# Kernel tuning notes

Hardware: AMD Instinct MI355X
Metric: run time of the kernel (lower is better)

Reference implementation:

```python
import jax, jax.numpy as jnp
import numpy as np

NUM_EMBEDDINGS = 1024
EMBEDDING_DIM = 256
COMMITMENT_COST = 0.25


def setup_inputs() -> dict:
    key = jax.random.key(0)
    k1, k2 = jax.random.split(key)
    z_e = jax.random.normal(k1, (32, 256, 32, 32), dtype=jnp.float32)
    # nn.init.uniform_(weight, -1/K, 1/K)
    bound = 1.0 / NUM_EMBEDDINGS
    weight = jax.random.uniform(k2, (NUM_EMBEDDINGS, EMBEDDING_DIM), dtype=jnp.float32,
                                minval=-bound, maxval=bound)
    return {"z_e": z_e, "weight": weight}


def reference(z_e, weight):
    B, C, H, W = z_e.shape
    sg = jax.lax.stop_gradient
    # (B, H, W, C) -> (N, C)
    flat = jnp.transpose(z_e, (0, 2, 3, 1)).reshape(-1, C)
    # squared L2 distances to each codebook vector: (N, K)
    dist = (jnp.sum(flat * flat, axis=1, keepdims=True)
            - 2.0 * flat @ weight.T
            + jnp.sum(weight * weight, axis=1))
    indices = jnp.argmin(dist, axis=1)  # (N,)
    # codebook lookup (equivalent to one-hot @ weight)
    quantized = weight[indices].reshape(B, H, W, C)
    quantized = jnp.transpose(quantized, (0, 3, 1, 2))  # (B, C, H, W)
    e_latent = jnp.mean((sg(quantized) - z_e) ** 2)
    q_latent = jnp.mean((quantized - sg(z_e)) ** 2)
    loss = q_latent + COMMITMENT_COST * e_latent
    # straight-through estimator
    quantized_st = z_e + sg(quantized - z_e)
    # codebook usage perplexity: avg_probs = mean of one-hot encodings
    n = flat.shape[0]
    counts = jax.ops.segment_sum(jnp.ones((n,), dtype=z_e.dtype), indices,
                                 num_segments=NUM_EMBEDDINGS)
    avg_probs = counts / n
    perplexity = jnp.exp(-jnp.sum(avg_probs * jnp.log(avg_probs + 1e-10)))
    return (quantized_st, loss, perplexity)
```

## Files before the change

### kernel.cpp

```cpp
#include <hip/hip_runtime.h>
#include <float.h>
#include <math.h>
#include <stdint.h>


#define NB   32
#define NC   256
#define NHW  1024
#define NK   1024
#define NELEM (NB*NC*NHW)

typedef __attribute__((ext_vector_type(8))) short bf16x8;
typedef __attribute__((ext_vector_type(4))) float f32x4;

__device__ __forceinline__ unsigned short f2bf(float f) {
    unsigned u = __float_as_uint(f);
    u += 0x7FFFu + ((u >> 16) & 1u);
    return (unsigned short)(u >> 16);
}

__global__ __launch_bounds__(256) void vq_prep(const float* __restrict__ w,
                                               unsigned short* __restrict__ cb,
                                               float* __restrict__ wsq,
                                               unsigned int* __restrict__ counts,
                                               float* __restrict__ loss_sum) {
    __shared__ float swsq[4][16];
    const int t   = blockIdx.x;
    const int tid = threadIdx.x;
    float sq = 0.f;
#pragma unroll
    for (int rep = 0; rep < 2; ++rep) {
        const int p = tid + rep * 256;
        const int cc = p >> 6, l = p & 63;
        const int n = l & 15, quad = l >> 4;
        const float* src = w + (t * 16 + n) * NC + cc * 32 + quad * 8;
        const float4 f0 = *(const float4*)src;
        const float4 f1 = *(const float4*)(src + 4);
        union { unsigned short u[8]; uint4 v; } pk;
        pk.u[0] = f2bf(-2.f * f0.x); pk.u[1] = f2bf(-2.f * f0.y);
        pk.u[2] = f2bf(-2.f * f0.z); pk.u[3] = f2bf(-2.f * f0.w);
        pk.u[4] = f2bf(-2.f * f1.x); pk.u[5] = f2bf(-2.f * f1.y);
        pk.u[6] = f2bf(-2.f * f1.z); pk.u[7] = f2bf(-2.f * f1.w);
        *(uint4*)(cb + (size_t)t * 4096 + cc * 512 + l * 8) = pk.v;
        sq = fmaf(f0.x, f0.x, sq); sq = fmaf(f0.y, f0.y, sq);
        sq = fmaf(f0.z, f0.z, sq); sq = fmaf(f0.w, f0.w, sq);
        sq = fmaf(f1.x, f1.x, sq); sq = fmaf(f1.y, f1.y, sq);
        sq = fmaf(f1.z, f1.z, sq); sq = fmaf(f1.w, f1.w, sq);
    }
    sq += __shfl_xor(sq, 16, 64);
    sq += __shfl_xor(sq, 32, 64);
    const int wv = tid >> 6, lane = tid & 63;
    if (lane < 16) swsq[wv][lane] = sq;
    __syncthreads();
    if (tid < 16)
        wsq[t * 16 + tid] = swsq[0][tid] + swsq[1][tid] + swsq[2][tid] + swsq[3][tid];
    if (t == 0) {
        for (int i = tid; i < NK; i += 256) counts[i] = 0u;
        if (tid == 0) loss_sum[0] = 0.f;
    }
}

__global__ __launch_bounds__(256, 2) void vq_dist(const float* __restrict__ z,
                                                  const float* __restrict__ wsq,
                                                  const unsigned short* __restrict__ cb,
                                                  unsigned int* __restrict__ counts,
                                                  int* __restrict__ gfidx) {
    __shared__ float sval[4][64];
    __shared__ int   sidx[4][64];

    const int tid  = threadIdx.x;
    const int wv   = tid >> 6;
    const int lane = tid & 63;
    const int n    = lane & 15;
    const int quad = lane >> 4;
    const int bid  = blockIdx.x;
    const int b    = bid >> 4;
    const int hw0  = (bid & 15) << 6;

    const float* zb = z + (size_t)b * (NC * NHW);

    bf16x8 bfr[4][8];
#pragma unroll
    for (int nt = 0; nt < 4; ++nt) {
#pragma unroll
        for (int cc = 0; cc < 8; ++cc) {
            const float* zp = zb + (size_t)(cc * 32 + quad * 8) * NHW + hw0 + nt * 16 + n;
            union { unsigned short u[8]; bf16x8 v; } pk;
#pragma unroll
            for (int j = 0; j < 8; ++j) pk.u[j] = f2bf(zp[(size_t)j * NHW]);
            bfr[nt][cc] = pk.v;
        }
    }

    float bv[4] = {FLT_MAX, FLT_MAX, FLT_MAX, FLT_MAX};
    int   bi[4] = {0, 0, 0, 0};
    const unsigned short* ap0 = cb + (size_t)(wv * 16) * 4096 + lane * 8;

    for (int mt = 0; mt < 16; ++mt) {
        const int kt = wv * 256 + mt * 16;
        const unsigned short* ap = ap0 + (size_t)mt * 4096;
        const f32x4 w4 = *(const f32x4*)(wsq + kt + quad * 4);
        f32x4 acc[4];
#pragma unroll
        for (int nt = 0; nt < 4; ++nt) acc[nt] = w4;
#pragma unroll
        for (int cc = 0; cc < 8; ++cc) {
            const bf16x8 af = *(const bf16x8*)(ap + cc * 512);
            acc[0] = __builtin_amdgcn_mfma_f32_16x16x32_bf16(af, bfr[0][cc], acc[0], 0, 0, 0);
            acc[1] = __builtin_amdgcn_mfma_f32_16x16x32_bf16(af, bfr[1][cc], acc[1], 0, 0, 0);
            acc[2] = __builtin_amdgcn_mfma_f32_16x16x32_bf16(af, bfr[2][cc], acc[2], 0, 0, 0);
            acc[3] = __builtin_amdgcn_mfma_f32_16x16x32_bf16(af, bfr[3][cc], acc[3], 0, 0, 0);
        }
#pragma unroll
        for (int nt = 0; nt < 4; ++nt) {
#pragma unroll
            for (int r = 0; r < 4; ++r) {
                const float v = acc[nt][r];
                if (v < bv[nt]) { bv[nt] = v; bi[nt] = kt + quad * 4 + r; }
            }
        }
    }

#pragma unroll
    for (int nt = 0; nt < 4; ++nt) {
#pragma unroll
        for (int off = 16; off <= 32; off <<= 1) {
            const float ov = __shfl_xor(bv[nt], off, 64);
            const int   ok = __shfl_xor(bi[nt], off, 64);
            if (ov < bv[nt] || (ov == bv[nt] && ok < bi[nt])) { bv[nt] = ov; bi[nt] = ok; }
        }
    }
    if (lane < 16) {
#pragma unroll
        for (int nt = 0; nt < 4; ++nt) {
            sval[wv][nt * 16 + lane] = bv[nt];
            sidx[wv][nt * 16 + lane] = bi[nt];
        }
    }
    __syncthreads();

    if (tid < 64) {
        float bestv = sval[0][tid];
        int   besti = sidx[0][tid];
#pragma unroll
        for (int q = 1; q < 4; ++q) {
            const float v = sval[q][tid];
            const int   k = sidx[q][tid];
            if (v < bestv || (v == bestv && k < besti)) { bestv = v; besti = k; }
        }
        gfidx[b * NHW + hw0 + tid] = besti;
        atomicAdd(&counts[besti], 1u);
    }
}

__global__ __launch_bounds__(256, 4) void vq_scatter(const float* __restrict__ z,
                                                     const float* __restrict__ w,
                                                     const int* __restrict__ gfidx,
                                                     float* __restrict__ loss_sum,
                                                     float* __restrict__ out) {
    __shared__ float lred[4];
    const int tid = threadIdx.x;
    const int bid = blockIdx.x;
    const int b   = bid >> 5;
    const int c0  = (bid & 31) << 3;
    const int hw4 = tid << 2;

    const int4 k4 = *(const int4*)(gfidx + b * NHW + hw4);
    const float* zb = z   + (size_t)b * (NC * NHW);
    float*       ob = out + (size_t)b * (NC * NHW);

    float lsum = 0.f;
#pragma unroll
    for (int i = 0; i < 8; ++i) {
        const int c = c0 + i;
        const float4 zq = *(const float4*)(zb + (size_t)c * NHW + hw4);
        float4 q;
        q.x = w[k4.x * NC + c];
        q.y = w[k4.y * NC + c];
        q.z = w[k4.z * NC + c];
        q.w = w[k4.w * NC + c];
        float d;
        d = q.x - zq.x; lsum = fmaf(d, d, lsum);
        d = q.y - zq.y; lsum = fmaf(d, d, lsum);
        d = q.z - zq.z; lsum = fmaf(d, d, lsum);
        d = q.w - zq.w; lsum = fmaf(d, d, lsum);
        *(float4*)(ob + (size_t)c * NHW + hw4) = q;
    }
#pragma unroll
    for (int off = 32; off; off >>= 1) lsum += __shfl_down(lsum, off, 64);
    const int lane = tid & 63, wv = tid >> 6;
    if (lane == 0) lred[wv] = lsum;
    __syncthreads();
    if (tid == 0)
        atomicAdd(loss_sum, lred[0] + lred[1] + lred[2] + lred[3]);
}

__global__ __launch_bounds__(256) void vq_final(const unsigned int* __restrict__ counts,
                                                const float* __restrict__ loss_sum,
                                                float* __restrict__ out) {
    __shared__ float red[4];
    const int tid = threadIdx.x;
    float s = 0.f;
#pragma unroll
    for (int p = 0; p < 4; ++p) {
        const float pr = (float)counts[tid + p * 256] * (1.f / 32768.f);
        s = fmaf(pr, logf(pr + 1e-10f), s);
    }
#pragma unroll
    for (int off = 32; off; off >>= 1) s += __shfl_down(s, off, 64);
    if ((tid & 63) == 0) red[tid >> 6] = s;
    __syncthreads();
    if (tid == 0) {
        const float tot = red[0] + red[1] + red[2] + red[3];
        out[NELEM]     = loss_sum[0] * (1.25f / (float)NELEM);
        out[NELEM + 1] = expf(-tot);
    }
}

extern "C" void kernel_launch(void* const* d_in, const int* in_sizes, int n_in,
                              void* d_out, int out_size, void* d_ws, size_t ws_size,
                              hipStream_t stream) {
    const float* z = (const float*)d_in[0];
    const float* w = (const float*)d_in[1];
    float* out = (float*)d_out;

    float*          wsq      = (float*)d_ws;
    unsigned int*   counts   = (unsigned int*)((char*)d_ws + 4096);
    float*          loss_sum = (float*)((char*)d_ws + 8192);
    unsigned short* cbfrag   = (unsigned short*)((char*)d_ws + 16384);
    int*            gfidx    = (int*)((char*)d_ws + 540672);

    vq_prep   <<<64,   256, 0, stream>>>(w, cbfrag, wsq, counts, loss_sum);
    vq_dist   <<<512,  256, 0, stream>>>(z, wsq, cbfrag, counts, gfidx);
    vq_scatter<<<1024, 256, 0, stream>>>(z, w, gfidx, loss_sum, out);
    vq_final  <<<1,    256, 0, stream>>>(counts, loss_sum, out);
}
```

Before: 138.2 us.

## Pre-pack z into bf16 MFMA fragments via LDS transpose kernel

```diff
diff --git a/kernel.cpp b/kernel.cpp
--- a/kernel.cpp
+++ b/kernel.cpp
@@ -60,14 +60,9 @@
     }
 }
 
-__global__ __launch_bounds__(256, 2) void vq_dist(const float* __restrict__ z,
-                                                  const float* __restrict__ wsq,
-                                                  const unsigned short* __restrict__ cb,
-                                                  unsigned int* __restrict__ counts,
-                                                  int* __restrict__ gfidx) {
-    __shared__ float sval[4][64];
-    __shared__ int   sidx[4][64];
-
+__global__ __launch_bounds__(256, 2) void vq_zpack(const float* __restrict__ z,
+                                                   unsigned short* __restrict__ zf) {
+    __shared__ float zt[256][66];
     const int tid  = threadIdx.x;
     const int wv   = tid >> 6;
     const int lane = tid & 63;
@@ -79,18 +74,54 @@
 
     const float* zb = z + (size_t)b * (NC * NHW);
 
+    {
+        const int hw4   = (tid & 15) * 4;
+        const int cbase = tid >> 4;
+#pragma unroll
+        for (int p = 0; p < 16; ++p) {
+            const int c = cbase + p * 16;
+            const float4 v = *(const float4*)(zb + (size_t)c * NHW + hw0 + hw4);
+            *(float2*)(&zt[c][hw4])     = make_float2(v.x, v.y);
+            *(float2*)(&zt[c][hw4 + 2]) = make_float2(v.z, v.w);
+        }
+    }
+    __syncthreads();
+
+    const size_t fb = (size_t)b * 64 + (hw0 >> 4) + wv;
+    unsigned short* dst0 = zf + fb * 4096;
+#pragma unroll
+    for (int cc = 0; cc < 8; ++cc) {
+        union { unsigned short u[8]; uint4 v; } pk;
+#pragma unroll
+        for (int j = 0; j < 8; ++j)
+            pk.u[j] = f2bf(zt[cc * 32 + quad * 8 + j][wv * 16 + n]);
+        *(uint4*)(dst0 + cc * 512 + lane * 8) = pk.v;
+    }
+}
+
+__global__ __launch_bounds__(256, 2) void vq_dist(const unsigned short* __restrict__ zf,
+                                                  const float* __restrict__ wsq,
+                                                  const unsigned short* __restrict__ cb,
+                                                  unsigned int* __restrict__ counts,
+                                                  int* __restrict__ gfidx) {
+    __shared__ float sval[4][64];
+    __shared__ int   sidx[4][64];
+
+    const int tid  = threadIdx.x;
+    const int wv   = tid >> 6;
+    const int lane = tid & 63;
+    const int quad = lane >> 4;
+    const int bid  = blockIdx.x;
+    const int b    = bid >> 4;
+    const int hw0  = (bid & 15) << 6;
+
+    const unsigned short* zf0 = zf + ((size_t)b * 64 + (hw0 >> 4)) * 4096 + lane * 8;
     bf16x8 bfr[4][8];
 #pragma unroll
-    for (int nt = 0; nt < 4; ++nt) {
-#pragma unroll
-        for (int cc = 0; cc < 8; ++cc) {
-            const float* zp = zb + (size_t)(cc * 32 + quad * 8) * NHW + hw0 + nt * 16 + n;
-            union { unsigned short u[8]; bf16x8 v; } pk;
-#pragma unroll
-            for (int j = 0; j < 8; ++j) pk.u[j] = f2bf(zp[(size_t)j * NHW]);
-            bfr[nt][cc] = pk.v;
-        }
-    }
+    for (int nt = 0; nt < 4; ++nt)
+#pragma unroll
+        for (int cc = 0; cc < 8; ++cc)
+            bfr[nt][cc] = *(const bf16x8*)(zf0 + (size_t)(nt * 8 + cc) * 512);
 
     float bv[4] = {FLT_MAX, FLT_MAX, FLT_MAX, FLT_MAX};
     int   bi[4] = {0, 0, 0, 0};
@@ -130,11 +161,12 @@
             if (ov < bv[nt] || (ov == bv[nt] && ok < bi[nt])) { bv[nt] = ov; bi[nt] = ok; }
         }
     }
+    const int n16 = lane & 15;
     if (lane < 16) {
 #pragma unroll
         for (int nt = 0; nt < 4; ++nt) {
-            sval[wv][nt * 16 + lane] = bv[nt];
-            sidx[wv][nt * 16 + lane] = bi[nt];
+            sval[wv][nt * 16 + n16] = bv[nt];
+            sidx[wv][nt * 16 + n16] = bi[nt];
         }
     }
     __syncthreads();
@@ -229,9 +261,11 @@
     float*          loss_sum = (float*)((char*)d_ws + 8192);
     unsigned short* cbfrag   = (unsigned short*)((char*)d_ws + 16384);
     int*            gfidx    = (int*)((char*)d_ws + 540672);
+    unsigned short* zfrag    = (unsigned short*)out;
 
     vq_prep   <<<64,   256, 0, stream>>>(w, cbfrag, wsq, counts, loss_sum);
-    vq_dist   <<<512,  256, 0, stream>>>(z, wsq, cbfrag, counts, gfidx);
+    vq_zpack  <<<512,  256, 0, stream>>>(z, zfrag);
+    vq_dist   <<<512,  256, 0, stream>>>(zfrag, wsq, cbfrag, counts, gfidx);
     vq_scatter<<<1024, 256, 0, stream>>>(z, w, gfidx, loss_sum, out);
     vq_final  <<<1,    256, 0, stream>>>(counts, loss_sum, out);
 }
```

Measured after the change: 144.4 us. 1.04x slower.
